# Performance work log

Measured on AMD Instinct MI355X. Metric: run time of the kernel, lower is better.

Reference implementation:

```python
import jax, jax.numpy as jnp
import numpy as np

N_NODES = 50000
N_EDGES = 500000
HEADS = 4
OUT_CH = 64
POS_DIM = 16
IN_CH = 256
DIVERSITY_WEIGHT = 0.1
NEG_SLOPE = 0.2


def setup_inputs() -> dict:
    key = jax.random.key(0)
    k = jax.random.split(key, 6)
    x = jax.random.normal(k[0], (N_NODES, IN_CH + POS_DIM), dtype=jnp.float32)
    # edges with no self-loops by construction (col = row + nonzero offset mod N)
    row = jax.random.randint(k[1], (N_EDGES,), 0, N_NODES)
    off = jax.random.randint(k[2], (N_EDGES,), 1, N_NODES)
    col = (row + off) % N_NODES
    edge_index = jnp.stack([row, col]).astype(jnp.int64)
    lin_w = jax.random.normal(k[3], (HEADS * OUT_CH, IN_CH), dtype=jnp.float32) * (1.0 / np.sqrt(IN_CH))
    att = jax.random.normal(k[4], (1, HEADS, 2 * OUT_CH), dtype=jnp.float32) * 0.1
    pos_att = jax.random.normal(k[5], (1, HEADS, 2 * POS_DIM), dtype=jnp.float32) * 0.1
    bias = jnp.zeros((HEADS * OUT_CH,), dtype=jnp.float32)
    return {"x": x, "edge_index": edge_index, "lin_w": lin_w, "att": att,
            "pos_att": pos_att, "bias": bias}


def _forward(x, edge_index, lin_w, att, pos_att, bias):
    N = x.shape[0]
    H, C = HEADS, OUT_CH
    pos = x[:, -POS_DIM:]              # [N, P]
    content_feat = x[:, :-POS_DIM]     # [N, IN_CH]
    content = (content_feat @ lin_w.T).reshape(N, H, C)  # [N, H, C]

    # add self loops (input edges contain none)
    sl = jnp.arange(N)
    row = jnp.concatenate([edge_index[0], sl])  # [E+N]
    col = jnp.concatenate([edge_index[1], sl])

    # cat([x_i, x_j]) * att summed == per-node split logits, gathered per edge
    a_src = jnp.einsum('nhc,hc->nh', content, att[0, :, :C])   # [N, H]
    a_dst = jnp.einsum('nhc,hc->nh', content, att[0, :, C:])
    p_src = pos @ pos_att[0, :, :POS_DIM].T                    # [N, H]
    p_dst = pos @ pos_att[0, :, POS_DIM:].T

    alpha = a_src[row] + a_dst[col] + p_src[row] + p_dst[col]  # [E+N, H]
    alpha = jax.nn.leaky_relu(alpha, NEG_SLOPE)

    # segment softmax over destination node (row), PyG-style with +1e-16
    amax = jax.ops.segment_max(alpha, row, num_segments=N)
    alpha = jnp.exp(alpha - amax[row])
    denom = jax.ops.segment_sum(alpha, row, num_segments=N)
    alpha = alpha / (denom[row] + 1e-16)

    # attention-head diversity loss: pairwise cosine similarity of alpha columns
    norms = jnp.maximum(jnp.sqrt(jnp.sum(alpha * alpha, axis=0)), 1e-8)  # [H]
    an = alpha / norms
    corr = an.T @ an                                            # [H, H]
    corr = corr * (1.0 - jnp.eye(H, dtype=corr.dtype))          # zero diagonal
    diversity_loss = jnp.mean(corr) * DIVERSITY_WEIGHT

    msgs = content[col] * alpha[:, :, None]                     # [E+N, H, C]
    out = jax.ops.segment_sum(msgs, row, num_segments=N)        # [N, H, C]
    out = out.reshape(N, H * C) + bias
    return out, diversity_loss


def reference(x, edge_index, lin_w, att, pos_att, bias):
    return _forward(x, edge_index, lin_w, att, pos_att, bias)
```

## Files before the change

### kernel.cpp

```cpp
#include <hip/hip_runtime.h>
#include <math.h>

#define NN 50000
#define NE 500000
#define HH 4
#define CC 64
#define HC 256
#define PD 16
#define XD 272
#define NEG 0.2f
#define SB 1024
#define NBLK (NN / 4)

typedef _Float16 half4 __attribute__((ext_vector_type(4)));
typedef _Float16 half8 __attribute__((ext_vector_type(8)));
typedef float floatx4 __attribute__((ext_vector_type(4)));

#define SA 40

__global__ void k_prep(const float* __restrict__ w, _Float16* __restrict__ wfrag,
                       int* __restrict__ counts) {
    int idx = blockIdx.x * blockDim.x + threadIdx.x;
    if (idx < NN) counts[idx] = 0;
    int j = idx & 7, lane = (idx >> 3) & 63, nt = (idx >> 9) & 3;
    int wv = (idx >> 11) & 3, kt = idx >> 13;
    int n = wv * 64 + nt * 16 + (lane & 15);
    int k = kt * 32 + (lane >> 4) * 8 + j;
    wfrag[idx] = (_Float16)w[(size_t)n * 256 + k];
}

__global__ __launch_bounds__(256) void k_gemm(const float* __restrict__ x,
                                              const _Float16* __restrict__ wfrag,
                                              const float* __restrict__ att,
                                              const float* __restrict__ patt,
                                              _Float16* __restrict__ content,
                                              float* __restrict__ ssrc,
                                              float* __restrict__ sdst) {
    __shared__ _Float16 As[64 * SA];
    const int tid = threadIdx.x;
    const int wv = tid >> 6, lane = tid & 63;
    const int nb = blockIdx.x * 64;
    const int m16 = lane & 15, q = lane >> 4;

    floatx4 acc[4][4];
#pragma unroll
    for (int mt = 0; mt < 4; mt++)
#pragma unroll
        for (int nt = 0; nt < 4; nt++) acc[mt][nt] = (floatx4){0.f, 0.f, 0.f, 0.f};

    const int arow = tid >> 2, akq = (tid & 3) * 8;
    const int anode = nb + arow;

#pragma unroll
    for (int kt = 0; kt < 8; kt++) {
        const int k0 = kt * 32;
        __syncthreads();
        float4 f0 = make_float4(0.f, 0.f, 0.f, 0.f), f1 = f0;
        if (anode < NN) {
            f0 = *(const float4*)&x[(size_t)anode * XD + k0 + akq];
            f1 = *(const float4*)&x[(size_t)anode * XD + k0 + akq + 4];
        }
        half8 hv;
        hv[0] = (_Float16)f0.x; hv[1] = (_Float16)f0.y;
        hv[2] = (_Float16)f0.z; hv[3] = (_Float16)f0.w;
        hv[4] = (_Float16)f1.x; hv[5] = (_Float16)f1.y;
        hv[6] = (_Float16)f1.z; hv[7] = (_Float16)f1.w;
        *(half8*)&As[arow * SA + akq] = hv;
        __syncthreads();

        half8 af[4], bf[4];
#pragma unroll
        for (int nt = 0; nt < 4; nt++)
            bf[nt] = *(const half8*)&wfrag[((((size_t)kt * 4 + wv) * 4 + nt) * 64 + lane) * 8];
#pragma unroll
        for (int mt = 0; mt < 4; mt++)
            af[mt] = *(half8*)&As[(mt * 16 + m16) * SA + q * 8];
#pragma unroll
        for (int mt = 0; mt < 4; mt++)
#pragma unroll
            for (int nt = 0; nt < 4; nt++)
                acc[mt][nt] = __builtin_amdgcn_mfma_f32_16x16x32_f16(
                    af[mt], bf[nt], acc[mt][nt], 0, 0, 0);
    }

    const int h = wv;
#pragma unroll
    for (int mt = 0; mt < 4; mt++) {
#pragma unroll
        for (int r = 0; r < 4; r++) {
            int node = nb + mt * 16 + q * 4 + r;
            if (node < NN) {
                float sa = 0.f, sb = 0.f;
#pragma unroll
                for (int nt = 0; nt < 4; nt++) {
                    float v = acc[mt][nt][r];
                    int cih = nt * 16 + m16;
                    content[(size_t)node * 256 + h * 64 + cih] = (_Float16)v;
                    sa += v * att[h * 128 + cih];
                    sb += v * att[h * 128 + 64 + cih];
                }
                float pv = x[(size_t)node * XD + 256 + m16];
                sa += pv * patt[h * 32 + m16];
                sb += pv * patt[h * 32 + 16 + m16];
#pragma unroll
                for (int m = 1; m < 16; m <<= 1) {
                    sa += __shfl_xor(sa, m, 64);
                    sb += __shfl_xor(sb, m, 64);
                }
                if (m16 == 0) {
                    ssrc[node * 4 + h] = sa;
                    sdst[node * 4 + h] = sb;
                }
            }
        }
    }
}

__global__ void k_count(const int* __restrict__ row, int* __restrict__ counts,
                        int* __restrict__ slot) {
    int e = blockIdx.x * blockDim.x + threadIdx.x;
    if (e < NE) slot[e] = atomicAdd(&counts[row[e]], 1);
}

__global__ __launch_bounds__(SB) void k_scan1(const int* __restrict__ counts, int* tmp, int* bsum) {
    __shared__ int s[SB];
    int i = blockIdx.x * SB + threadIdx.x;
    int v = (i < NN) ? counts[i] : 0;
    s[threadIdx.x] = v;
    __syncthreads();
    for (int off = 1; off < SB; off <<= 1) {
        int t = (threadIdx.x >= off) ? s[threadIdx.x - off] : 0;
        __syncthreads();
        s[threadIdx.x] += t;
        __syncthreads();
    }
    if (i < NN) tmp[i] = s[threadIdx.x];
    if (threadIdx.x == SB - 1) bsum[blockIdx.x] = s[SB - 1];
}

__global__ void k_scan2(const int* __restrict__ bsum, int* __restrict__ bcar, int nb) {
    int lane = threadIdx.x;
    int v = (lane < nb) ? bsum[lane] : 0;
#pragma unroll
    for (int off = 1; off < 64; off <<= 1) {
        int t = __shfl_up(v, off);
        if (lane >= off) v += t;
    }
    if (lane < nb) bcar[lane] = v - bsum[lane];
}

__global__ void k_scan3(const int* tmp, const int* counts, const int* bcar, int* off) {
    int i = blockIdx.x * blockDim.x + threadIdx.x;
    if (i < NN) off[i] = tmp[i] - counts[i] + bcar[i / SB];
}

__global__ void k_place(const int* __restrict__ row, const int* __restrict__ col,
                        const int* __restrict__ offs, const int* __restrict__ slot,
                        int* __restrict__ sorted) {
    int e = blockIdx.x * blockDim.x + threadIdx.x;
    if (e < NE) sorted[offs[row[e]] + slot[e]] = col[e];
}

__global__ __launch_bounds__(256) void k_node(const _Float16* __restrict__ content,
                                              const float* __restrict__ ssrc,
                                              const float* __restrict__ sdst,
                                              const int* __restrict__ counts,
                                              const int* __restrict__ off,
                                              const int* __restrict__ sorted,
                                              const float* __restrict__ bias,
                                              float* __restrict__ out,
                                              float* __restrict__ gpart) {
    __shared__ float gsh[16];
    __shared__ float ash[4][64][4];
    __shared__ int   csh[4][64];
    const int w = threadIdx.x >> 6;
    const int lane = threadIdx.x & 63;
    const int n = blockIdx.x * 4 + w;
    if (threadIdx.x < 16) gsh[threadIdx.x] = 0.f;
    __syncthreads();

    const int cnt = counts[n], base = off[n];
    const int total = cnt + 1;
    const float4 ss = *(const float4*)&ssrc[n * 4];
    const int hsel = lane >> 4;
    const half4* c4 = (const half4*)content;

    float4 acc = make_float4(0.f, 0.f, 0.f, 0.f);
    float g[10];
#pragma unroll
    for (int k = 0; k < 10; k++) g[k] = 0.f;

    if (total <= 64) {
        const int l = lane;
        const bool act = (l < total);
        const int c = (l < cnt) ? sorted[base + l] : n;
        float4 sd = *(const float4*)&sdst[c * 4];
        float r0 = ss.x + sd.x; r0 = r0 > 0.f ? r0 : NEG * r0;
        float r1 = ss.y + sd.y; r1 = r1 > 0.f ? r1 : NEG * r1;
        float r2 = ss.z + sd.z; r2 = r2 > 0.f ? r2 : NEG * r2;
        float r3 = ss.w + sd.w; r3 = r3 > 0.f ? r3 : NEG * r3;
        float m0 = act ? r0 : -1e30f, m1 = act ? r1 : -1e30f;
        float m2 = act ? r2 : -1e30f, m3 = act ? r3 : -1e30f;
#pragma unroll
        for (int s = 1; s < 64; s <<= 1) {
            m0 = fmaxf(m0, __shfl_xor(m0, s));
            m1 = fmaxf(m1, __shfl_xor(m1, s));
            m2 = fmaxf(m2, __shfl_xor(m2, s));
            m3 = fmaxf(m3, __shfl_xor(m3, s));
        }
        float e0 = act ? __expf(r0 - m0) : 0.f;
        float e1 = act ? __expf(r1 - m1) : 0.f;
        float e2 = act ? __expf(r2 - m2) : 0.f;
        float e3 = act ? __expf(r3 - m3) : 0.f;
        float s0 = e0, s1 = e1, s2 = e2, s3 = e3;
#pragma unroll
        for (int s = 1; s < 64; s <<= 1) {
            s0 += __shfl_xor(s0, s); s1 += __shfl_xor(s1, s);
            s2 += __shfl_xor(s2, s); s3 += __shfl_xor(s3, s);
        }
        float a0 = e0 / (s0 + 1e-16f), a1 = e1 / (s1 + 1e-16f);
        float a2 = e2 / (s2 + 1e-16f), a3 = e3 / (s3 + 1e-16f);

        g[0] = a0 * a0; g[1] = a0 * a1; g[2] = a0 * a2; g[3] = a0 * a3;
        g[4] = a1 * a1; g[5] = a1 * a2; g[6] = a1 * a3;
        g[7] = a2 * a2; g[8] = a2 * a3; g[9] = a3 * a3;

        ash[w][l][0] = a0; ash[w][l][1] = a1;
        ash[w][l][2] = a2; ash[w][l][3] = a3;
        csh[w][l] = c;

        const int nit = (total + 15) & ~15;
        for (int e = 0; e < nit; e += 16) {
            int   ci[16];
            float bi[16];
#pragma unroll
            for (int u = 0; u < 16; u++) {
                ci[u] = csh[w][e + u];
                bi[u] = ash[w][e + u][hsel];
            }
            half4 vi[16];
#pragma unroll
            for (int u = 0; u < 16; u++) vi[u] = c4[(size_t)ci[u] * 64 + lane];
#pragma unroll
            for (int u = 0; u < 16; u++) {
                acc.x += bi[u] * (float)vi[u][0];
                acc.y += bi[u] * (float)vi[u][1];
                acc.z += bi[u] * (float)vi[u][2];
                acc.w += bi[u] * (float)vi[u][3];
            }
        }
    } else {
        const int nch = (total + 63) >> 6;
        float m0 = -1e30f, m1 = -1e30f, m2 = -1e30f, m3 = -1e30f;
        for (int ch = 0; ch < nch; ch++) {
            int l = ch * 64 + lane;
            if (l < total) {
                int c = (l < cnt) ? sorted[base + l] : n;
                float4 sd = *(const float4*)&sdst[c * 4];
                float r0 = ss.x + sd.x; r0 = r0 > 0.f ? r0 : NEG * r0;
                float r1 = ss.y + sd.y; r1 = r1 > 0.f ? r1 : NEG * r1;
                float r2 = ss.z + sd.z; r2 = r2 > 0.f ? r2 : NEG * r2;
                float r3 = ss.w + sd.w; r3 = r3 > 0.f ? r3 : NEG * r3;
                m0 = fmaxf(m0, r0); m1 = fmaxf(m1, r1);
                m2 = fmaxf(m2, r2); m3 = fmaxf(m3, r3);
            }
        }
#pragma unroll
        for (int s = 1; s < 64; s <<= 1) {
            m0 = fmaxf(m0, __shfl_xor(m0, s));
            m1 = fmaxf(m1, __shfl_xor(m1, s));
            m2 = fmaxf(m2, __shfl_xor(m2, s));
            m3 = fmaxf(m3, __shfl_xor(m3, s));
        }
        float s0 = 0.f, s1 = 0.f, s2 = 0.f, s3 = 0.f;
        for (int ch = 0; ch < nch; ch++) {
            int l = ch * 64 + lane;
            if (l < total) {
                int c = (l < cnt) ? sorted[base + l] : n;
                float4 sd = *(const float4*)&sdst[c * 4];
                float r0 = ss.x + sd.x; r0 = r0 > 0.f ? r0 : NEG * r0;
                float r1 = ss.y + sd.y; r1 = r1 > 0.f ? r1 : NEG * r1;
                float r2 = ss.z + sd.z; r2 = r2 > 0.f ? r2 : NEG * r2;
                float r3 = ss.w + sd.w; r3 = r3 > 0.f ? r3 : NEG * r3;
                s0 += __expf(r0 - m0); s1 += __expf(r1 - m1);
                s2 += __expf(r2 - m2); s3 += __expf(r3 - m3);
            }
        }
#pragma unroll
        for (int s = 1; s < 64; s <<= 1) {
            s0 += __shfl_xor(s0, s); s1 += __shfl_xor(s1, s);
            s2 += __shfl_xor(s2, s); s3 += __shfl_xor(s3, s);
        }
        const float i0 = 1.f / (s0 + 1e-16f), i1 = 1.f / (s1 + 1e-16f);
        const float i2 = 1.f / (s2 + 1e-16f), i3 = 1.f / (s3 + 1e-16f);

        for (int ch = 0; ch < nch; ch++) {
            int l = ch * 64 + lane;
            int c = n;
            float a0 = 0.f, a1 = 0.f, a2 = 0.f, a3 = 0.f;
            if (l < total) {
                c = (l < cnt) ? sorted[base + l] : n;
                float4 sd = *(const float4*)&sdst[c * 4];
                float r0 = ss.x + sd.x; r0 = r0 > 0.f ? r0 : NEG * r0;
                float r1 = ss.y + sd.y; r1 = r1 > 0.f ? r1 : NEG * r1;
                float r2 = ss.z + sd.z; r2 = r2 > 0.f ? r2 : NEG * r2;
                float r3 = ss.w + sd.w; r3 = r3 > 0.f ? r3 : NEG * r3;
                a0 = __expf(r0 - m0) * i0; a1 = __expf(r1 - m1) * i1;
                a2 = __expf(r2 - m2) * i2; a3 = __expf(r3 - m3) * i3;
            }
            g[0] += a0 * a0; g[1] += a0 * a1; g[2] += a0 * a2; g[3] += a0 * a3;
            g[4] += a1 * a1; g[5] += a1 * a2; g[6] += a1 * a3;
            g[7] += a2 * a2; g[8] += a2 * a3; g[9] += a3 * a3;

            int cc = min(64, total - ch * 64);
            for (int e = 0; e < cc; e++) {
                float b0 = __shfl(a0, e), b1 = __shfl(a1, e);
                float b2 = __shfl(a2, e), b3 = __shfl(a3, e);
                int ce = __shfl(c, e);
                float mya = hsel == 0 ? b0 : hsel == 1 ? b1 : hsel == 2 ? b2 : b3;
                half4 cv = c4[(size_t)ce * 64 + lane];
                acc.x += mya * (float)cv[0]; acc.y += mya * (float)cv[1];
                acc.z += mya * (float)cv[2]; acc.w += mya * (float)cv[3];
            }
        }
    }

    float4 bv = ((const float4*)bias)[lane];
    acc.x += bv.x; acc.y += bv.y; acc.z += bv.z; acc.w += bv.w;
    ((float4*)out)[(size_t)n * 64 + lane] = acc;

#pragma unroll
    for (int s = 1; s < 64; s <<= 1) {
#pragma unroll
        for (int k = 0; k < 10; k++) g[k] += __shfl_xor(g[k], s);
    }
    if (lane == 0) {
#pragma unroll
        for (int k = 0; k < 10; k++) atomicAdd(&gsh[k], g[k]);
    }
    __syncthreads();
    if (threadIdx.x < 10) gpart[(size_t)blockIdx.x * 10 + threadIdx.x] = gsh[threadIdx.x];
}

__global__ __launch_bounds__(1024) void k_final(const float* __restrict__ gpart,
                                                float* __restrict__ out_div) {
    __shared__ float s[1024];
    const int t = threadIdx.x;
    const int k = t & 15, grp = t >> 4;
    float v = 0.f;
    if (k < 10) {
        for (int b = grp; b < NBLK; b += 64) v += gpart[(size_t)b * 10 + k];
    }
    s[t] = v;
    __syncthreads();
    for (int off = 512; off >= 16; off >>= 1) {
        if (t < off) s[t] += s[t + off];
        __syncthreads();
    }
    if (t == 0) {
        float g00 = s[0], g01 = s[1], g02 = s[2], g03 = s[3];
        float g11 = s[4], g12 = s[5], g13 = s[6];
        float g22 = s[7], g23 = s[8], g33 = s[9];
        float n0 = fmaxf(sqrtf(g00), 1e-8f), n1 = fmaxf(sqrtf(g11), 1e-8f);
        float n2 = fmaxf(sqrtf(g22), 1e-8f), n3 = fmaxf(sqrtf(g33), 1e-8f);
        float sum = g01 / (n0 * n1) + g02 / (n0 * n2) + g03 / (n0 * n3) +
                    g12 / (n1 * n2) + g13 / (n1 * n3) + g23 / (n2 * n3);
        sum *= 2.0f;
        out_div[0] = sum / 16.0f * 0.1f;
    }
}

extern "C" void kernel_launch(void* const* d_in, const int* in_sizes, int n_in,
                              void* d_out, int out_size, void* d_ws, size_t ws_size,
                              hipStream_t stream) {
    const float* x    = (const float*)d_in[0];
    const int*   ei   = (const int*)d_in[1];
    const int*   row  = ei;
    const int*   col  = ei + NE;
    const float* w    = (const float*)d_in[2];
    const float* att  = (const float*)d_in[3];
    const float* patt = (const float*)d_in[4];
    const float* bias = (const float*)d_in[5];
    float* out = (float*)d_out;

    char* p = (char*)d_ws;
    _Float16* content = (_Float16*)p; p += (size_t)NN * 256 * 2;
    _Float16* wfrag   = (_Float16*)p; p += (size_t)256 * 256 * 2;
    float* ssrc    = (float*)p; p += (size_t)NN * 4 * 4;
    float* sdst    = (float*)p; p += (size_t)NN * 4 * 4;
    float* gpart   = (float*)p; p += (size_t)NBLK * 10 * 4;
    int* counts    = (int*)p;   p += (size_t)NN * 4;
    int* offs      = (int*)p;   p += (size_t)NN * 4;
    int* tmp       = (int*)p;   p += (size_t)NN * 4;
    int* bsum      = (int*)p;   p += 64 * 4;
    int* bcar      = (int*)p;   p += 64 * 4;
    int* slot      = (int*)p;   p += (size_t)NE * 4;
    int* sorted    = (int*)p;   p += (size_t)NE * 4;

    k_prep<<<256, 256, 0, stream>>>(w, wfrag, counts);

    k_count<<<(NE + 255) / 256, 256, 0, stream>>>(row, counts, slot);

    k_gemm<<<(NN + 63) / 64, 256, 0, stream>>>(x, wfrag, att, patt, content, ssrc, sdst);

    int nb1 = (NN + SB - 1) / SB;
    k_scan1<<<nb1, SB, 0, stream>>>(counts, tmp, bsum);
    k_scan2<<<1, 64, 0, stream>>>(bsum, bcar, nb1);
    k_scan3<<<(NN + 255) / 256, 256, 0, stream>>>(tmp, counts, bcar, offs);
    k_place<<<(NE + 255) / 256, 256, 0, stream>>>(row, col, offs, slot, sorted);

    k_node<<<NBLK, 256, 0, stream>>>(content, ssrc, sdst, counts, offs, sorted,
                                     bias, out, gpart);
    k_final<<<1, 1024, 0, stream>>>(gpart, out + (size_t)NN * 256);
}
```

Before: 304.4 us.

## Load GEMM A fragments from global directly, merge scan kernels, shrink gather unroll

The GEMM no longer stages x tiles through shared memory with two barriers per k-step. Each lane now loads and converts its own A fragment straight from global memory. The three-kernel prefix scan is replaced by one kernel that gives each block a base offset from a global atomic counter. Segments stay contiguous per node but are no longer in node order, which is fine because consumers index through offs. The k_node gather unroll drops from 16 to 8, which cuts register pressure and padding waste at the cost of less memory-level parallelism.

New measurement: 305.3 us. No clear change (+0.3%).

```diff
diff --git a/kernel.cpp b/kernel.cpp
--- a/kernel.cpp
+++ b/kernel.cpp
@@ -16,12 +16,11 @@
 typedef _Float16 half8 __attribute__((ext_vector_type(8)));
 typedef float floatx4 __attribute__((ext_vector_type(4)));
 
-#define SA 40
-
 __global__ void k_prep(const float* __restrict__ w, _Float16* __restrict__ wfrag,
-                       int* __restrict__ counts) {
+                       int* __restrict__ counts, int* __restrict__ gcur) {
     int idx = blockIdx.x * blockDim.x + threadIdx.x;
     if (idx < NN) counts[idx] = 0;
+    if (idx == NN) *gcur = 0;
     int j = idx & 7, lane = (idx >> 3) & 63, nt = (idx >> 9) & 3;
     int wv = (idx >> 11) & 3, kt = idx >> 13;
     int n = wv * 64 + nt * 16 + (lane & 15);
@@ -36,7 +35,6 @@
                                               _Float16* __restrict__ content,
                                               float* __restrict__ ssrc,
                                               float* __restrict__ sdst) {
-    __shared__ _Float16 As[64 * SA];
     const int tid = threadIdx.x;
     const int wv = tid >> 6, lane = tid & 63;
     const int nb = blockIdx.x * 64;
@@ -48,33 +46,32 @@
 #pragma unroll
         for (int nt = 0; nt < 4; nt++) acc[mt][nt] = (floatx4){0.f, 0.f, 0.f, 0.f};
 
-    const int arow = tid >> 2, akq = (tid & 3) * 8;
-    const int anode = nb + arow;
+    const float* xr[4];
+#pragma unroll
+    for (int mt = 0; mt < 4; mt++) {
+        int node = nb + mt * 16 + m16;
+        if (node >= NN) node = NN - 1;
+        xr[mt] = &x[(size_t)node * XD + q * 8];
+    }
 
 #pragma unroll
     for (int kt = 0; kt < 8; kt++) {
-        const int k0 = kt * 32;
-        __syncthreads();
-        float4 f0 = make_float4(0.f, 0.f, 0.f, 0.f), f1 = f0;
-        if (anode < NN) {
-            f0 = *(const float4*)&x[(size_t)anode * XD + k0 + akq];
-            f1 = *(const float4*)&x[(size_t)anode * XD + k0 + akq + 4];
-        }
-        half8 hv;
-        hv[0] = (_Float16)f0.x; hv[1] = (_Float16)f0.y;
-        hv[2] = (_Float16)f0.z; hv[3] = (_Float16)f0.w;
-        hv[4] = (_Float16)f1.x; hv[5] = (_Float16)f1.y;
-        hv[6] = (_Float16)f1.z; hv[7] = (_Float16)f1.w;
-        *(half8*)&As[arow * SA + akq] = hv;
-        __syncthreads();
-
-        half8 af[4], bf[4];
+        half8 bf[4];
 #pragma unroll
         for (int nt = 0; nt < 4; nt++)
             bf[nt] = *(const half8*)&wfrag[((((size_t)kt * 4 + wv) * 4 + nt) * 64 + lane) * 8];
-#pragma unroll
-        for (int mt = 0; mt < 4; mt++)
-            af[mt] = *(half8*)&As[(mt * 16 + m16) * SA + q * 8];
+        half8 af[4];
+#pragma unroll
+        for (int mt = 0; mt < 4; mt++) {
+            float4 f0 = *(const float4*)(xr[mt] + kt * 32);
+            float4 f1 = *(const float4*)(xr[mt] + kt * 32 + 4);
+            half8 hv;
+            hv[0] = (_Float16)f0.x; hv[1] = (_Float16)f0.y;
+            hv[2] = (_Float16)f0.z; hv[3] = (_Float16)f0.w;
+            hv[4] = (_Float16)f1.x; hv[5] = (_Float16)f1.y;
+            hv[6] = (_Float16)f1.z; hv[7] = (_Float16)f1.w;
+            af[mt] = hv;
+        }
 #pragma unroll
         for (int mt = 0; mt < 4; mt++)
 #pragma unroll
@@ -122,8 +119,11 @@
     if (e < NE) slot[e] = atomicAdd(&counts[row[e]], 1);
 }
 
-__global__ __launch_bounds__(SB) void k_scan1(const int* __restrict__ counts, int* tmp, int* bsum) {
+__global__ __launch_bounds__(SB) void k_offs(const int* __restrict__ counts,
+                                             int* __restrict__ offs,
+                                             int* __restrict__ gcur) {
     __shared__ int s[SB];
+    __shared__ int basesh;
     int i = blockIdx.x * SB + threadIdx.x;
     int v = (i < NN) ? counts[i] : 0;
     s[threadIdx.x] = v;
@@ -134,24 +134,9 @@
         s[threadIdx.x] += t;
         __syncthreads();
     }
-    if (i < NN) tmp[i] = s[threadIdx.x];
-    if (threadIdx.x == SB - 1) bsum[blockIdx.x] = s[SB - 1];
-}
-
-__global__ void k_scan2(const int* __restrict__ bsum, int* __restrict__ bcar, int nb) {
-    int lane = threadIdx.x;
-    int v = (lane < nb) ? bsum[lane] : 0;
-#pragma unroll
-    for (int off = 1; off < 64; off <<= 1) {
-        int t = __shfl_up(v, off);
-        if (lane >= off) v += t;
-    }
-    if (lane < nb) bcar[lane] = v - bsum[lane];
-}
-
-__global__ void k_scan3(const int* tmp, const int* counts, const int* bcar, int* off) {
-    int i = blockIdx.x * blockDim.x + threadIdx.x;
-    if (i < NN) off[i] = tmp[i] - counts[i] + bcar[i / SB];
+    if (threadIdx.x == SB - 1) basesh = atomicAdd(gcur, s[SB - 1]);
+    __syncthreads();
+    if (i < NN) offs[i] = basesh + s[threadIdx.x] - v;
 }
 
 __global__ void k_place(const int* __restrict__ row, const int* __restrict__ col,
@@ -229,20 +214,20 @@
         ash[w][l][2] = a2; ash[w][l][3] = a3;
         csh[w][l] = c;
 
-        const int nit = (total + 15) & ~15;
-        for (int e = 0; e < nit; e += 16) {
-            int   ci[16];
-            float bi[16];
-#pragma unroll
-            for (int u = 0; u < 16; u++) {
+        const int nit = (total + 7) & ~7;
+        for (int e = 0; e < nit; e += 8) {
+            int   ci[8];
+            float bi[8];
+#pragma unroll
+            for (int u = 0; u < 8; u++) {
                 ci[u] = csh[w][e + u];
                 bi[u] = ash[w][e + u][hsel];
             }
-            half4 vi[16];
-#pragma unroll
-            for (int u = 0; u < 16; u++) vi[u] = c4[(size_t)ci[u] * 64 + lane];
-#pragma unroll
-            for (int u = 0; u < 16; u++) {
+            half4 vi[8];
+#pragma unroll
+            for (int u = 0; u < 8; u++) vi[u] = c4[(size_t)ci[u] * 64 + lane];
+#pragma unroll
+            for (int u = 0; u < 8; u++) {
                 acc.x += bi[u] * (float)vi[u][0];
                 acc.y += bi[u] * (float)vi[u][1];
                 acc.z += bi[u] * (float)vi[u][2];
@@ -391,22 +376,18 @@
     float* gpart   = (float*)p; p += (size_t)NBLK * 10 * 4;
     int* counts    = (int*)p;   p += (size_t)NN * 4;
     int* offs      = (int*)p;   p += (size_t)NN * 4;
-    int* tmp       = (int*)p;   p += (size_t)NN * 4;
-    int* bsum      = (int*)p;   p += 64 * 4;
-    int* bcar      = (int*)p;   p += 64 * 4;
+    int* gcur      = (int*)p;   p += 64;
     int* slot      = (int*)p;   p += (size_t)NE * 4;
     int* sorted    = (int*)p;   p += (size_t)NE * 4;
 
-    k_prep<<<256, 256, 0, stream>>>(w, wfrag, counts);
+    k_prep<<<256, 256, 0, stream>>>(w, wfrag, counts, gcur);
 
     k_count<<<(NE + 255) / 256, 256, 0, stream>>>(row, counts, slot);
 
     k_gemm<<<(NN + 63) / 64, 256, 0, stream>>>(x, wfrag, att, patt, content, ssrc, sdst);
 
     int nb1 = (NN + SB - 1) / SB;
-    k_scan1<<<nb1, SB, 0, stream>>>(counts, tmp, bsum);
-    k_scan2<<<1, 64, 0, stream>>>(bsum, bcar, nb1);
-    k_scan3<<<(NN + 255) / 256, 256, 0, stream>>>(tmp, counts, bcar, offs);
+    k_offs<<<nb1, SB, 0, stream>>>(counts, offs, gcur);
     k_place<<<(NE + 255) / 256, 256, 0, stream>>>(row, col, offs, slot, sorted);
 
     k_node<<<NBLK, 256, 0, stream>>>(content, ssrc, sdst, counts, offs, sorted,
```
